# Performance work log

Hardware: AMD Instinct MI355X
Metric: run time of the kernel (lower is better)

Reference implementation:

```python
import jax, jax.numpy as jnp
import numpy as np

EMBED_DIM = 1024
NUM_HEADS = 16
HEAD_DIM = EMBED_DIM // NUM_HEADS


def setup_inputs() -> dict:
    key = jax.random.key(0)
    ks = jax.random.split(key, 11)
    B, S, D = 4, 2048, EMBED_DIM
    s = 1.0 / np.sqrt(D)
    return {
        "query": jax.random.normal(ks[0], (B, S, D), jnp.float32),
        "key": jax.random.normal(ks[1], (B, S, D), jnp.float32),
        "value": jax.random.normal(ks[2], (B, S, D), jnp.float32),
        "Wq": jax.random.normal(ks[3], (D, D), jnp.float32) * s,
        "bq": jnp.zeros((D,), jnp.float32),
        "Wk": jax.random.normal(ks[4], (D, D), jnp.float32) * s,
        "bk": jnp.zeros((D,), jnp.float32),
        "Wv": jax.random.normal(ks[5], (D, D), jnp.float32) * s,
        "bv": jnp.zeros((D,), jnp.float32),
        "Wo": jax.random.normal(ks[6], (D, D), jnp.float32) * s,
        "bo": jnp.zeros((D,), jnp.float32),
    }


def _split_heads(x):
    B, S, D = x.shape
    return x.reshape(B, S, NUM_HEADS, HEAD_DIM).transpose(0, 2, 1, 3)  # (B,H,S,hd)


def reference(query, key, value, Wq, bq, Wk, bk, Wv, bv, Wo, bo):
    q = _split_heads(query @ Wq + bq)
    k = _split_heads(key @ Wk + bk)
    v = _split_heads(value @ Wv + bv)
    # naive scaled dot-product attention: full (B,H,S,S) scores materialized
    scores = jnp.einsum("bhqd,bhkd->bhqk", q, k) / np.sqrt(HEAD_DIM).astype(np.float32)
    attn = jax.nn.softmax(scores, axis=-1)
    ctx = jnp.einsum("bhqk,bhkd->bhqd", attn, v)
    B, H, S, hd = ctx.shape
    ctx = ctx.transpose(0, 2, 1, 3).reshape(B, S, H * hd)
    return ctx @ Wo + bo
```

## Files before the change

kernel.cpp:

```cpp
#include <hip/hip_runtime.h>

typedef unsigned short u16;
typedef unsigned int u32;
typedef _Float16 f16;
typedef __attribute__((ext_vector_type(8))) _Float16 f16x8;
typedef __attribute__((ext_vector_type(4))) float f32x4;
typedef __attribute__((ext_vector_type(4))) u32 u32x4;
typedef __attribute__((ext_vector_type(2))) u32 u32x2;
typedef __attribute__((ext_vector_type(4))) u16 u16x4;

static __device__ __forceinline__ u16 f16r(float f) {
  return __builtin_bit_cast(u16, (_Float16)f);
}
static __device__ __forceinline__ u32 packh(float a, float b) {
  return __builtin_bit_cast(u32, __builtin_amdgcn_cvt_pkrtz(a, b));
}
static __device__ __forceinline__ void gload16(const u16* g, u16* l) {
  __builtin_amdgcn_global_load_lds((const __attribute__((address_space(1))) void*)g,
                                   (__attribute__((address_space(3))) void*)l, 16, 0, 0);
}
static __device__ __forceinline__ void gload16f(const float* g, float* l) {
  __builtin_amdgcn_global_load_lds((const __attribute__((address_space(1))) void*)g,
                                   (__attribute__((address_space(3))) void*)l, 16, 0, 0);
}

__global__ __launch_bounds__(256) void wtrans4_k(
    const float* __restrict__ Wq, const float* __restrict__ Wk,
    const float* __restrict__ Wv, const float* __restrict__ Wo,
    u16* __restrict__ Tq, u16* __restrict__ Tk, u16* __restrict__ Tv, u16* __restrict__ To) {
  int z = blockIdx.z;
  const float* W = z == 0 ? Wq : z == 1 ? Wk : z == 2 ? Wv : Wo;
  u16* WT = z == 0 ? Tq : z == 1 ? Tk : z == 2 ? Tv : To;
  __shared__ float tile[32][33];
  int k0 = blockIdx.x * 32, n0 = blockIdx.y * 32;
  int t = threadIdx.x;
  int r = t >> 3, c = (t & 7) * 4;
  f32x4 v = *(const f32x4*)&W[(size_t)(k0 + r) * 1024 + n0 + c];
  tile[r][c + 0] = v[0]; tile[r][c + 1] = v[1]; tile[r][c + 2] = v[2]; tile[r][c + 3] = v[3];
  __syncthreads();
  int n = n0 + (t >> 3), kbase = k0 + (t & 7) * 4;
  u16x4 o;
#pragma unroll
  for (int j = 0; j < 4; j++) o[j] = f16r(tile[(t & 7) * 4 + j][t >> 3]);
  int nt = n >> 7, row = n & 127;
  int kt = kbase >> 5, lc = (kbase >> 3) & 3, e = kbase & 7;
  int pc = lc ^ (row & 3);
  *(u16x4*)&WT[((size_t)(nt * 32 + kt) * 128 + row) * 32 + pc * 8 + e] = o;
}

__global__ __launch_bounds__(256) void gemm_qkv_k(
    const float* __restrict__ Aq, const float* __restrict__ Ak, const float* __restrict__ Av,
    const u16* __restrict__ Tq, const u16* __restrict__ Tk, const u16* __restrict__ Tv,
    const float* __restrict__ bq, const float* __restrict__ bk, const float* __restrict__ bv,
    u16* __restrict__ Qo, u16* __restrict__ Ko, u16* __restrict__ Vo, float qscale) {
  int z = blockIdx.z;
  const float* A = z == 0 ? Aq : z == 1 ? Ak : Av;
  const u16* BT = z == 0 ? Tq : z == 1 ? Tk : Tv;
  const float* bias = z == 0 ? bq : z == 1 ? bk : bv;
  u16* out = z == 0 ? Qo : z == 1 ? Ko : Vo;
  int vmode = (z == 2);
  float scale = z == 0 ? qscale : 1.0f;

  __shared__ float As[2][128 * 32];
  __shared__ u16 Bs[2][128 * 32];
  int lid = blockIdx.x;
  int xcd = lid & 7, idx = lid >> 3;
  int bx = idx & 7, by = xcd * 8 + (idx >> 3);
  int n0 = bx * 128, m0 = by * 128;
  int tid = threadIdx.x, lane = tid & 63;
  int w = tid >> 6, wr = w >> 1, wc = w & 1;
  int fq = lane & 15, fc = lane >> 4;
  f32x4 acc[4][4] = {};
  const u16* BTb = BT + (size_t)bx * 131072;

  auto stage = [&](int ks, int sel) {
    const float* Ab = A + (size_t)m0 * 1024 + ks * 32;
#pragma unroll
    for (int i = 0; i < 4; i++) {
      int u = (w * 4 + i) * 64 + lane;
      int row = u >> 3, pc = u & 7;
      int koff = (pc ^ (row & 7)) << 2;
      gload16f(Ab + (size_t)row * 1024 + koff, &As[sel][(w * 4 + i) * 256]);
    }
    const u16* Bt = BTb + ks * 4096;
#pragma unroll
    for (int i = 0; i < 2; i++)
      gload16(Bt + (w * 2 + i) * 512 + lane * 8, &Bs[sel][(w * 2 + i) * 512]);
  };

  stage(0, 0);
  __syncthreads();
#pragma unroll 2
  for (int ks = 0; ks < 32; ks++) {
    int cur = ks & 1;
    if (ks < 31) stage(ks + 1, cur ^ 1);
    f16x8 af[4], bfv[4];
#pragma unroll
    for (int mi = 0; mi < 4; mi++) {
      int row = wr * 64 + mi * 16 + fq;
      int pc0 = (2 * fc) ^ (row & 7);
      f32x4 x0 = *(const f32x4*)&As[cur][row * 32 + pc0 * 4];
      f32x4 x1 = *(const f32x4*)&As[cur][row * 32 + (pc0 ^ 1) * 4];
      u32x4 pk = {packh(x0[0], x0[1]), packh(x0[2], x0[3]),
                  packh(x1[0], x1[1]), packh(x1[2], x1[3])};
      af[mi] = __builtin_bit_cast(f16x8, pk);
    }
#pragma unroll
    for (int ni = 0; ni < 4; ni++) {
      int row = wc * 64 + ni * 16 + fq;
      bfv[ni] = *(const f16x8*)&Bs[cur][row * 32 + (fc ^ (row & 3)) * 8];
    }
    __builtin_amdgcn_s_setprio(1);
#pragma unroll
    for (int mi = 0; mi < 4; mi++)
#pragma unroll
      for (int ni = 0; ni < 4; ni++)
        acc[mi][ni] = __builtin_amdgcn_mfma_f32_16x16x32_f16(af[mi], bfv[ni], acc[mi][ni], 0, 0, 0);
    __builtin_amdgcn_s_setprio(0);
    __syncthreads();
  }
#pragma unroll
  for (int mi = 0; mi < 4; mi++)
#pragma unroll
    for (int ni = 0; ni < 4; ni++) {
      int n = n0 + wc * 64 + ni * 16 + fq;
      float bs = bias[n];
      int h = n >> 6, d = n & 63;
#pragma unroll
      for (int r = 0; r < 4; r++) {
        int m = m0 + wr * 64 + mi * 16 + fc * 4 + r;
        int b = m >> 11, s = m & 2047;
        float v = (acc[mi][ni][r] + bs) * scale;
        size_t o;
        if (vmode == 0) {
          int t = s >> 4, fqo = s & 15, kco = d >> 5, fco = (d & 31) >> 3, e = d & 7;
          o = (size_t)(b * 16 + h) * 131072 + (size_t)((((t * 2 + kco) * 64) + fco * 16 + fqo) * 8 + e);
        } else {
          int kvc = s >> 5, dt = d >> 4, fqo = d & 15, fco = (s & 31) >> 3, e = s & 7;
          o = (size_t)(b * 16 + h) * 131072 + (size_t)((((kvc * 4 + dt) * 64) + fco * 16 + fqo) * 8 + e);
        }
        out[o] = f16r(v);
      }
    }
}

__global__ __launch_bounds__(256) void gemm_o_k(
    const u16* __restrict__ Ag, const u16* __restrict__ Bg,
    const float* __restrict__ bias, float* __restrict__ out) {
  __shared__ u16 SA[2][8192];
  __shared__ u16 SB[2][8192];
  int lid = blockIdx.x;
  int xcd = lid & 7, idx = lid >> 3;
  int bx = idx & 7, by = xcd * 8 + (idx >> 3);
  int n0 = bx * 128, m0 = by * 128;
  int tid = threadIdx.x, lane = tid & 63;
  int w = tid >> 6, wr = w >> 1, wc = w & 1;
  int fq = lane & 15, fc = lane >> 4;
  f32x4 acc[4][4] = {};

  auto stage = [&](int ks, int sel) {
    size_t at = ((size_t)by * 16 + ks) * 8192;
    size_t bt = ((size_t)bx * 32 + ks * 2) * 4096;
#pragma unroll
    for (int i = 0; i < 4; i++) {
      int ub = (w * 4 + i) * 512;
      gload16(Ag + at + ub + lane * 8, &SA[sel][ub]);
      gload16(Bg + bt + ub + lane * 8, &SB[sel][ub]);
    }
  };

  stage(0, 0);
  __syncthreads();
#pragma unroll 2
  for (int ks = 0; ks < 16; ks++) {
    int cur = ks & 1;
    if (ks < 15) stage(ks + 1, cur ^ 1);
#pragma unroll
    for (int kc = 0; kc < 2; kc++) {
      f16x8 ah[4], bh[4];
#pragma unroll
      for (int mi = 0; mi < 4; mi++) {
        int row = wr * 64 + mi * 16 + fq;
        ah[mi] = *(const f16x8*)&SA[cur][row * 64 + (((kc * 4 + fc) ^ (row & 7)) << 3)];
      }
#pragma unroll
      for (int ni = 0; ni < 4; ni++) {
        int row = wc * 64 + ni * 16 + fq;
        bh[ni] = *(const f16x8*)&SB[cur][kc * 4096 + row * 32 + (fc ^ (row & 3)) * 8];
      }
      __builtin_amdgcn_s_setprio(1);
#pragma unroll
      for (int mi = 0; mi < 4; mi++)
#pragma unroll
        for (int ni = 0; ni < 4; ni++)
          acc[mi][ni] = __builtin_amdgcn_mfma_f32_16x16x32_f16(ah[mi], bh[ni], acc[mi][ni], 0, 0, 0);
      __builtin_amdgcn_s_setprio(0);
    }
    __syncthreads();
  }
#pragma unroll
  for (int mi = 0; mi < 4; mi++)
#pragma unroll
    for (int ni = 0; ni < 4; ni++) {
      int n = n0 + wc * 64 + ni * 16 + fq;
      float bs = bias[n];
#pragma unroll
      for (int r = 0; r < 4; r++) {
        int m = m0 + wr * 64 + mi * 16 + fc * 4 + r;
        out[(size_t)m * 1024 + n] = acc[mi][ni][r] + bs;
      }
    }
}

__global__ __launch_bounds__(512) void attn_k(
    const u16* __restrict__ Q, const u16* __restrict__ Kg, const u16* __restrict__ Vg,
    u16* __restrict__ ctx) {
  int lid = blockIdx.x;
  int bh = (lid & 7) * 8 + (lid >> 6);
  int qb = (lid >> 3) & 7;
  int tid = threadIdx.x, lane = tid & 63, w = tid >> 6;
  const u16* Qf = Q + (size_t)bh * 131072;
  const u16* Kf = Kg + (size_t)bh * 131072;
  const u16* Vf = Vg + (size_t)bh * 131072;
  int fq = lane & 15, fc = lane >> 4;
  int le = lane * 8;
  int q0 = qb * 256 + w * 32;

  __shared__ u16 KL[2][4096];
  __shared__ u16 VL[2][4096];
  __shared__ u16 P[8][1152];

  f16x8 qf[2][2];
#pragma unroll
  for (int mi = 0; mi < 2; mi++)
#pragma unroll
    for (int kc = 0; kc < 2; kc++)
      qf[mi][kc] = *(const f16x8*)&Qf[((((q0 + 16 * mi) >> 4) * 2 + kc) << 9) + le];

  f32x4 O[2][4] = {};
  float lrow[2] = {0.f, 0.f};

  auto stage = [&](int tt, int bb) {
    int qo = (w & 3) * 1024;
    if (w < 4) {
      const u16* Kt = Kf + tt * 4096;
      gload16(Kt + qo + le, &KL[bb][qo]);
      gload16(Kt + qo + 512 + le, &KL[bb][qo + 512]);
    } else {
      const u16* Vt = Vf + tt * 4096;
      gload16(Vt + qo + le, &VL[bb][qo]);
      gload16(Vt + qo + 512 + le, &VL[bb][qo + 512]);
    }
  };

  stage(0, 0);
  __syncthreads();

  for (int t = 0; t < 32; t++) {
    int buf = t & 1;
    if (t < 31) stage(t + 1, buf ^ 1);

    f16x8 kf[8];
#pragma unroll
    for (int c = 0; c < 8; c++) kf[c] = *(const f16x8*)&KL[buf][c * 512 + le];

    f32x4 sc[2][4] = {};
    __builtin_amdgcn_s_setprio(1);
#pragma unroll
    for (int mi = 0; mi < 2; mi++)
#pragma unroll
      for (int sub = 0; sub < 4; sub++)
#pragma unroll
        for (int kc = 0; kc < 2; kc++)
          sc[mi][sub] = __builtin_amdgcn_mfma_f32_16x16x32_f16(kf[sub * 2 + kc], qf[mi][kc],
                                                               sc[mi][sub], 0, 0, 0);
    __builtin_amdgcn_s_setprio(0);

    f16x8 vf[8];
#pragma unroll
    for (int c = 0; c < 8; c++) vf[c] = *(const f16x8*)&VL[buf][c * 512 + le];

#pragma unroll
    for (int mi = 0; mi < 2; mi++) {
      float lloc = 0.f;
#pragma unroll
      for (int sub = 0; sub < 4; sub++) {
        float p0 = __builtin_amdgcn_exp2f(sc[mi][sub][0]);
        float p1 = __builtin_amdgcn_exp2f(sc[mi][sub][1]);
        float p2 = __builtin_amdgcn_exp2f(sc[mi][sub][2]);
        float p3 = __builtin_amdgcn_exp2f(sc[mi][sub][3]);
        lloc += (p0 + p1) + (p2 + p3);
        u32x2 pw = {packh(p0, p1), packh(p2, p3)};
        *(u32x2*)&P[w][fq * 72 + sub * 16 + fc * 4] = pw;
      }
      lloc += __shfl_xor(lloc, 16);
      lloc += __shfl_xor(lloc, 32);
      lrow[mi] += lloc;

      asm volatile("s_waitcnt lgkmcnt(0)" ::: "memory");
      __builtin_amdgcn_s_setprio(1);
#pragma unroll
      for (int ch = 0; ch < 2; ch++) {
        f16x8 pa = *(const f16x8*)&P[w][fq * 72 + ch * 32 + fc * 8];
#pragma unroll
        for (int db = 0; db < 4; db++)
          O[mi][db] = __builtin_amdgcn_mfma_f32_16x16x32_f16(pa, vf[ch * 4 + db], O[mi][db], 0, 0, 0);
      }
      __builtin_amdgcn_s_setprio(0);
    }

    __syncthreads();
  }

  int b = bh >> 4, h = bh & 15;
#pragma unroll
  for (int mi = 0; mi < 2; mi++) {
    float linv[4];
#pragma unroll
    for (int r = 0; r < 4; r++) linv[r] = 1.0f / __shfl(lrow[mi], fc * 4 + r);
#pragma unroll
    for (int db = 0; db < 4; db++)
#pragma unroll
      for (int r = 0; r < 4; r++) {
        float v = O[mi][db][r] * linv[r];
        int s = q0 + mi * 16 + fc * 4 + r;
        int mrow = s & 127, mt = b * 16 + (s >> 7);
        int lc = (db * 16 + fq) >> 3, e = fq & 7;
        int pc = lc ^ (mrow & 7);
        size_t o = ((size_t)(mt * 16 + h) * 128 + mrow) * 64 + pc * 8 + e;
        ctx[o] = f16r(v);
      }
  }
}

extern "C" void kernel_launch(void* const* d_in, const int* in_sizes, int n_in,
                              void* d_out, int out_size, void* d_ws, size_t ws_size,
                              hipStream_t stream) {
  const float* query = (const float*)d_in[0];
  const float* key   = (const float*)d_in[1];
  const float* value = (const float*)d_in[2];
  const float* Wq = (const float*)d_in[3];
  const float* bq = (const float*)d_in[4];
  const float* Wk = (const float*)d_in[5];
  const float* bk = (const float*)d_in[6];
  const float* Wv = (const float*)d_in[7];
  const float* bv = (const float*)d_in[8];
  const float* Wo = (const float*)d_in[9];
  const float* bo = (const float*)d_in[10];
  float* out = (float*)d_out;

  char* ws = (char*)d_ws;
  size_t off = 0;
  auto alloc = [&](size_t bytes) {
    char* p = ws + off;
    off += (bytes + 255) & ~(size_t)255;
    return p;
  };
  u16* WqT = (u16*)alloc(1048576 * 2);
  u16* WkT = (u16*)alloc(1048576 * 2);
  u16* WvT = (u16*)alloc(1048576 * 2);
  u16* WoT = (u16*)alloc(1048576 * 2);
  u16* Qbf = (u16*)alloc((size_t)8388608 * 2);
  u16* Kbf = (u16*)alloc((size_t)8388608 * 2);
  u16* ctx = (u16*)alloc((size_t)8388608 * 2);
  u16* Vfb = (u16*)d_out;

  const float QSCALE = 0.125f * 1.44269504f;

  wtrans4_k<<<dim3(32, 32, 4), 256, 0, stream>>>(Wq, Wk, Wv, Wo, WqT, WkT, WvT, WoT);
  gemm_qkv_k<<<dim3(512, 1, 3), 256, 0, stream>>>(query, key, value, WqT, WkT, WvT,
                                                  bq, bk, bv, Qbf, Kbf, Vfb, QSCALE);
  attn_k<<<512, 512, 0, stream>>>(Qbf, Kbf, Vfb, ctx);
  gemm_o_k<<<512, 256, 0, stream>>>(ctx, WoT, bo, out);
}
```

Baseline: 194.0 us.

## Prefetch two stages ahead with explicit vmcnt waits and change B-tile swizzle

The three kernels (QKV GEMM, output GEMM, attention) now issue loads two K-steps ahead into the double buffer. Each iteration waits with a partial s_waitcnt vmcnt instead of a full __syncthreads, so global loads for the next stage stay in flight across the barrier. Raw s_barrier and sched_barrier replace the old syncs to pin instruction ordering. The weight-transpose swizzle and the matching B-fragment reads change from row&3 to (row>>1)&3 to cut LDS bank conflicts. The hand-counted vmcnt values must match the exact number of loads per stage, or the kernels read stale shared memory.

Result: no change. 192.8 us (-0.6%).

```diff
diff --git a/kernel.cpp b/kernel.cpp
--- a/kernel.cpp
+++ b/kernel.cpp
@@ -44,7 +44,7 @@
   for (int j = 0; j < 4; j++) o[j] = f16r(tile[(t & 7) * 4 + j][t >> 3]);
   int nt = n >> 7, row = n & 127;
   int kt = kbase >> 5, lc = (kbase >> 3) & 3, e = kbase & 7;
-  int pc = lc ^ (row & 3);
+  int pc = lc ^ ((row >> 1) & 3);
   *(u16x4*)&WT[((size_t)(nt * 32 + kt) * 128 + row) * 32 + pc * 8 + e] = o;
 }
 
@@ -89,11 +89,13 @@
   };
 
   stage(0, 0);
-  __syncthreads();
-#pragma unroll 2
+  stage(1, 1);
   for (int ks = 0; ks < 32; ks++) {
     int cur = ks & 1;
-    if (ks < 31) stage(ks + 1, cur ^ 1);
+    if (ks < 31) asm volatile("s_waitcnt vmcnt(6)" ::: "memory");
+    else         asm volatile("s_waitcnt vmcnt(0)" ::: "memory");
+    __builtin_amdgcn_s_barrier();
+    __builtin_amdgcn_sched_barrier(0);
     f16x8 af[4], bfv[4];
 #pragma unroll
     for (int mi = 0; mi < 4; mi++) {
@@ -108,7 +110,7 @@
 #pragma unroll
     for (int ni = 0; ni < 4; ni++) {
       int row = wc * 64 + ni * 16 + fq;
-      bfv[ni] = *(const f16x8*)&Bs[cur][row * 32 + (fc ^ (row & 3)) * 8];
+      bfv[ni] = *(const f16x8*)&Bs[cur][row * 32 + (fc ^ ((row >> 1) & 3)) * 8];
     }
     __builtin_amdgcn_s_setprio(1);
 #pragma unroll
@@ -117,7 +119,9 @@
       for (int ni = 0; ni < 4; ni++)
         acc[mi][ni] = __builtin_amdgcn_mfma_f32_16x16x32_f16(af[mi], bfv[ni], acc[mi][ni], 0, 0, 0);
     __builtin_amdgcn_s_setprio(0);
-    __syncthreads();
+    __builtin_amdgcn_sched_barrier(0);
+    __builtin_amdgcn_s_barrier();
+    if (ks < 30) stage(ks + 2, cur);
   }
 #pragma unroll
   for (int mi = 0; mi < 4; mi++)
@@ -170,11 +174,13 @@
   };
 
   stage(0, 0);
-  __syncthreads();
-#pragma unroll 2
+  stage(1, 1);
   for (int ks = 0; ks < 16; ks++) {
     int cur = ks & 1;
-    if (ks < 15) stage(ks + 1, cur ^ 1);
+    if (ks < 15) asm volatile("s_waitcnt vmcnt(8)" ::: "memory");
+    else         asm volatile("s_waitcnt vmcnt(0)" ::: "memory");
+    __builtin_amdgcn_s_barrier();
+    __builtin_amdgcn_sched_barrier(0);
 #pragma unroll
     for (int kc = 0; kc < 2; kc++) {
       f16x8 ah[4], bh[4];
@@ -186,7 +192,7 @@
 #pragma unroll
       for (int ni = 0; ni < 4; ni++) {
         int row = wc * 64 + ni * 16 + fq;
-        bh[ni] = *(const f16x8*)&SB[cur][kc * 4096 + row * 32 + (fc ^ (row & 3)) * 8];
+        bh[ni] = *(const f16x8*)&SB[cur][kc * 4096 + row * 32 + (fc ^ ((row >> 1) & 3)) * 8];
       }
       __builtin_amdgcn_s_setprio(1);
 #pragma unroll
@@ -196,7 +202,9 @@
           acc[mi][ni] = __builtin_amdgcn_mfma_f32_16x16x32_f16(ah[mi], bh[ni], acc[mi][ni], 0, 0, 0);
       __builtin_amdgcn_s_setprio(0);
     }
-    __syncthreads();
+    __builtin_amdgcn_sched_barrier(0);
+    __builtin_amdgcn_s_barrier();
+    if (ks < 14) stage(ks + 2, cur);
   }
 #pragma unroll
   for (int mi = 0; mi < 4; mi++)
@@ -254,11 +262,13 @@
   };
 
   stage(0, 0);
-  __syncthreads();
-
+  stage(1, 1);
   for (int t = 0; t < 32; t++) {
     int buf = t & 1;
-    if (t < 31) stage(t + 1, buf ^ 1);
+    if (t < 31) asm volatile("s_waitcnt vmcnt(2)" ::: "memory");
+    else        asm volatile("s_waitcnt vmcnt(0)" ::: "memory");
+    __builtin_amdgcn_s_barrier();
+    __builtin_amdgcn_sched_barrier(0);
 
     f16x8 kf[8];
 #pragma unroll
@@ -298,6 +308,7 @@
       lrow[mi] += lloc;
 
       asm volatile("s_waitcnt lgkmcnt(0)" ::: "memory");
+      __builtin_amdgcn_sched_barrier(0);
       __builtin_amdgcn_s_setprio(1);
 #pragma unroll
       for (int ch = 0; ch < 2; ch++) {
@@ -309,7 +320,9 @@
       __builtin_amdgcn_s_setprio(0);
     }
 
-    __syncthreads();
+    __builtin_amdgcn_sched_barrier(0);
+    __builtin_amdgcn_s_barrier();
+    if (t < 30) stage(t + 2, buf);
   }
 
   int b = bh >> 4, h = bh & 15;
```
